# Optimization experiments

Measured on AMD Instinct MI355X. Metric: run time of the kernel, lower is better.

## Reference

```python
import jax, jax.numpy as jnp
import numpy as np

B, C, H, W = 4, 256, 200, 200
N_ROIS = 2048
CROP = 7
NUM_CLASSES = 2
HID = 1024
FAN_IN = C * CROP * CROP


def _linear_params(key, fan_in, fan_out):
    s = 1.0 / np.sqrt(fan_in)
    kw, kb = jax.random.split(key)
    w = jax.random.uniform(kw, (fan_out, fan_in), jnp.float32, -s, s)
    b = jax.random.uniform(kb, (fan_out,), jnp.float32, -s, s)
    return w, b


def setup_inputs() -> dict:
    key = jax.random.key(0)
    ks = jax.random.split(key, 10)
    x = jax.random.normal(ks[0], (B, C, H, W), jnp.float32)
    # rois: (batch_idx, x1, y1, x2, y2) in feature-map coords, sizes ~4-22px
    bi = jax.random.randint(ks[1], (N_ROIS,), 0, B).astype(jnp.float32)
    x1 = jax.random.uniform(ks[2], (N_ROIS,)) * (W - 24)
    y1 = jax.random.uniform(ks[3], (N_ROIS,)) * (H - 24)
    x2 = x1 + 4.0 + jax.random.uniform(ks[4], (N_ROIS,)) * 18.0
    y2 = y1 + 4.0 + jax.random.uniform(ks[5], (N_ROIS,)) * 18.0
    rpn_rois = jnp.stack([bi, x1, y1, x2, y2], axis=1)
    w1, b1 = _linear_params(ks[6], FAN_IN, HID)
    w2, b2 = _linear_params(ks[7], HID, HID)
    wc, bc = _linear_params(ks[8], HID, NUM_CLASSES)
    wb, bb = _linear_params(ks[9], HID, NUM_CLASSES * 4)
    return {"x": x, "rpn_rois": rpn_rois, "w1": w1, "b1": b1,
            "w2": w2, "b2": b2, "wc": wc, "bc": bc, "wb": wb, "bb": bb}


def roi_align(x, rois):
    """Per-ROI bilinear crop (RoIAlign, 1 sample/bin). x:[B,C,H,W], rois:[N,5] -> [N, C*CROP*CROP]."""
    n = rois.shape[0]
    b = rois[:, 0].astype(jnp.int32)
    rx1, ry1, rx2, ry2 = rois[:, 1], rois[:, 2], rois[:, 3], rois[:, 4]
    bw = (rx2 - rx1) / CROP
    bh = (ry2 - ry1) / CROP
    c = jnp.arange(CROP, dtype=jnp.float32) + 0.5  # bin centers
    sx = rx1[:, None] + c[None, :] * bw[:, None]   # [N, CROP]
    sy = ry1[:, None] + c[None, :] * bh[:, None]   # [N, CROP]
    P = CROP * CROP
    px = jnp.broadcast_to(sx[:, None, :], (n, CROP, CROP)).reshape(n, P)
    py = jnp.broadcast_to(sy[:, :, None], (n, CROP, CROP)).reshape(n, P)
    px = jnp.clip(px, 0.0, W - 1)
    py = jnp.clip(py, 0.0, H - 1)
    x0 = jnp.floor(px).astype(jnp.int32)
    y0 = jnp.floor(py).astype(jnp.int32)
    x1i = jnp.minimum(x0 + 1, W - 1)
    y1i = jnp.minimum(y0 + 1, H - 1)
    wx = (px - x0.astype(px.dtype))[..., None]  # [N,P,1]
    wy = (py - y0.astype(py.dtype))[..., None]
    be = jnp.broadcast_to(b[:, None], (n, P))
    v00 = x[be, :, y0, x0]   # [N,P,C] irregular gathers
    v01 = x[be, :, y0, x1i]
    v10 = x[be, :, y1i, x0]
    v11 = x[be, :, y1i, x1i]
    val = (v00 * (1 - wy) * (1 - wx) + v01 * (1 - wy) * wx
           + v10 * wy * (1 - wx) + v11 * wy * wx)        # [N,P,C]
    return val.transpose(0, 2, 1).reshape(n, C * P)       # channel-major flatten, matches torch


def reference(x, rpn_rois, w1, b1, w2, b2, wc, bc, wb, bb):
    crops = roi_align(x, rpn_rois)                 # [N, C*cs*cs]
    h = jax.nn.relu(crops @ w1.T + b1)             # fc1
    h = jax.nn.relu(h @ w2.T + b2)                 # fc2
    rcnn_class_logits = h @ wc.T + bc              # [N, num_classes]
    rcnn_bbox = h @ wb.T + bb                      # [N, num_classes*4]
    return (rcnn_class_logits, rcnn_bbox)
```

## Files before the change

### kernel.cpp

```cpp
#include <hip/hip_runtime.h>

#define NROI  2048
#define CCH   256
#define IMH   200
#define IMW   200
#define CROP  7
#define PP    49
#define FANIN 12544
#define HID   1024

typedef _Float16 f16x8 __attribute__((ext_vector_type(8)));
typedef _Float16 f16x4 __attribute__((ext_vector_type(4)));
typedef __attribute__((ext_vector_type(4))) float f32x4;

__device__ __forceinline__ void gload16(const void* g, void* l) {
    __builtin_amdgcn_global_load_lds(
        (const __attribute__((address_space(1))) void*)g,
        (__attribute__((address_space(3))) void*)l, 16, 0, 0);
}

__global__ __launch_bounds__(256) void transpose_f16(
    const float* __restrict__ x, _Float16* __restrict__ xT)
{
    __shared__ _Float16 t[100][258];

    const int half = blockIdx.x;
    const int h    = blockIdx.y;
    const int b    = blockIdx.z;
    const int c    = threadIdx.x;

    const float* src = x + ((size_t)(b * CCH + c) * IMH + h) * IMW + half * 100;
#pragma unroll
    for (int i = 0; i < 25; ++i) {
        const float4 v = *(const float4*)(src + i * 4);
        t[i * 4 + 0][c] = (_Float16)v.x;
        t[i * 4 + 1][c] = (_Float16)v.y;
        t[i * 4 + 2][c] = (_Float16)v.z;
        t[i * 4 + 3][c] = (_Float16)v.w;
    }
    __syncthreads();

    _Float16* dst = xT + ((size_t)(b * IMH + h) * IMW + half * 100) * CCH;
    const int wq = threadIdx.x >> 5;
    const int l32 = threadIdx.x & 31;
#pragma unroll
    for (int r = 0; r < 13; ++r) {
        const int w = r * 8 + wq;
        if (w < 100)
            *(f16x8*)(dst + (size_t)w * CCH + l32 * 8) =
                *(const f16x8*)&t[w][l32 * 8];
    }
}

__global__ __launch_bounds__(256) void roi_gather_kernel(
    const _Float16* __restrict__ xT, const float* __restrict__ rois,
    _Float16* __restrict__ crops)
{
    const int n    = blockIdx.x;
    const int wave = threadIdx.x >> 6;
    const int lane = threadIdx.x & 63;

    const int   b   = (int)rois[(size_t)n * 5 + 0];
    const float rx1 = rois[(size_t)n * 5 + 1];
    const float ry1 = rois[(size_t)n * 5 + 2];
    const float rx2 = rois[(size_t)n * 5 + 3];
    const float ry2 = rois[(size_t)n * 5 + 4];
    const float bw = (rx2 - rx1) / 7.0f;
    const float bh = (ry2 - ry1) / 7.0f;

    const _Float16* xb = xT + (size_t)b * (IMH * IMW * CCH);
    _Float16* crow = crops + (size_t)n * FANIN;

    for (int p = wave; p < PP; p += 4) {
        const int i = p / 7;
        const int j = p - i * 7;
        float px = __fadd_rn(rx1, __fmul_rn((float)j + 0.5f, bw));
        float py = __fadd_rn(ry1, __fmul_rn((float)i + 0.5f, bh));
        px = fminf(fmaxf(px, 0.0f), (float)(IMW - 1));
        py = fminf(fmaxf(py, 0.0f), (float)(IMH - 1));
        const float fx = floorf(px), fy = floorf(py);
        const int x0 = (int)fx, y0 = (int)fy;
        const int dxo = (min(x0 + 1, IMW - 1) - x0) * CCH;
        const int dyo = (min(y0 + 1, IMH - 1) - y0) * (IMW * CCH);
        const float wx = px - fx, wy = py - fy;

        const _Float16* cb = xb + (size_t)(y0 * IMW + x0) * CCH + lane * 4;
        const f16x4 A = *(const f16x4*)(cb);
        const f16x4 B = *(const f16x4*)(cb + dxo);
        const f16x4 C = *(const f16x4*)(cb + dyo);
        const f16x4 D = *(const f16x4*)(cb + dyo + dxo);

        f16x4 o;
#pragma unroll
        for (int e = 0; e < 4; ++e) {
            const float v00 = (float)A[e], v01 = (float)B[e];
            const float v10 = (float)C[e], v11 = (float)D[e];
            const float top = v00 + wx * (v01 - v00);
            const float bot = v10 + wx * (v11 - v10);
            o[e] = (_Float16)(top + wy * (bot - top));
        }
        *(f16x4*)(crow + p * CCH + lane * 4) = o;
    }
}

__global__ __launch_bounds__(256) void permute_w1_kernel(
    const float* __restrict__ w1, _Float16* __restrict__ w1P)
{
    __shared__ _Float16 row[FANIN];

    const int o   = blockIdx.x;
    const int tid = threadIdx.x;
    const float* src = w1 + (size_t)o * FANIN;

    for (int g = tid; g < FANIN / 4; g += 256) {
        const float4 v = *(const float4*)(src + g * 4);
        f16x4 f = {(_Float16)v.x, (_Float16)v.y, (_Float16)v.z, (_Float16)v.w};
        *(f16x4*)&row[g * 4] = f;
    }
    __syncthreads();

    _Float16* dst = w1P + (size_t)o * FANIN;
    for (int g = tid; g < FANIN; g += 256) {
        const int p = g >> 8;
        const int c = g & 255;
        dst[g] = row[c * PP + p];
    }
}

__global__ __launch_bounds__(256) void convert_f16(
    const float* __restrict__ w, _Float16* __restrict__ wF, int n4)
{
    for (int g = blockIdx.x * 256 + threadIdx.x; g < n4; g += gridDim.x * 256) {
        const float4 v = ((const float4*)w)[g];
        f16x4 o = {(_Float16)v.x, (_Float16)v.y, (_Float16)v.z, (_Float16)v.w};
        ((f16x4*)wF)[g] = o;
    }
}

__global__ __launch_bounds__(512, 1) void gemm_f16_256(
    const _Float16* __restrict__ A, const _Float16* __restrict__ B,
    float* __restrict__ P, int M, int N, int K, int kLen)
{
    __shared__ _Float16 lds[2][2][256][64];

    const int flat = blockIdx.x;
    const int xcd  = flat & 7;
    const int idx  = flat >> 3;
    const int bn4  = xcd & 3;
    const int half = xcd >> 2;
    const int bm8  = half * 4 + (idx & 3);
    const int z    = idx >> 2;

    const int tid  = threadIdx.x;
    const int wave = tid >> 6;
    const int lane = tid & 63;
    const int bm = bm8 * 256;
    const int bn = bn4 * 256;
    const int kBase = z * kLen;
    const int wr = wave >> 1;
    const int wc = wave & 1;

    f32x4 acc[4][8];
#pragma unroll
    for (int i = 0; i < 4; ++i)
#pragma unroll
        for (int j = 0; j < 8; ++j) acc[i][j] = (f32x4){0.f, 0.f, 0.f, 0.f};

    const int r_st = wave * 32 + (lane >> 3);
    const int s_st = ((lane & 7) ^ ((lane >> 4) & 3)) * 8;
    const _Float16* gA = A + (size_t)(bm + r_st) * K + kBase + s_st;
    const _Float16* gB = B + (size_t)(bn + r_st) * K + kBase + s_st;
    const size_t rstep8 = (size_t)8 * K;

    const int li = lane & 15;
    const int hi = lane >> 4;
    const int swb = (li >> 1) & 3;

    {
        _Float16* dA = &lds[0][0][wave * 32][0];
        _Float16* dB = &lds[0][1][wave * 32][0];
#pragma unroll
        for (int ck = 0; ck < 4; ++ck) {
            gload16(gA + ck * rstep8, dA + ck * 512);
            gload16(gB + ck * rstep8, dB + ck * 512);
        }
    }
    __syncthreads();

    int cur = 0;
    for (int kt = 0; kt < kLen; kt += 64) {
        if (kt + 64 < kLen) {
            _Float16* dA = &lds[cur ^ 1][0][wave * 32][0];
            _Float16* dB = &lds[cur ^ 1][1][wave * 32][0];
#pragma unroll
            for (int ck = 0; ck < 4; ++ck) {
                gload16(gA + kt + 64 + ck * rstep8, dA + ck * 512);
                gload16(gB + kt + 64 + ck * rstep8, dB + ck * 512);
            }
        }

#pragma unroll
        for (int kk = 0; kk < 2; ++kk) {
            const int sw = (((kk << 2) | hi) ^ swb) * 8;
            f16x8 a[4], b[8];
#pragma unroll
            for (int m = 0; m < 4; ++m)
                a[m] = *(const f16x8*)&lds[cur][0][wr * 64 + m * 16 + li][sw];
#pragma unroll
            for (int n = 0; n < 8; ++n)
                b[n] = *(const f16x8*)&lds[cur][1][wc * 128 + n * 16 + li][sw];
#pragma unroll
            for (int m = 0; m < 4; ++m)
#pragma unroll
                for (int n = 0; n < 8; ++n)
                    acc[m][n] = __builtin_amdgcn_mfma_f32_16x16x32_f16(a[m], b[n], acc[m][n], 0, 0, 0);
        }
        __syncthreads();
        cur ^= 1;
    }

    float* Pz = P + (size_t)z * M * N;
#pragma unroll
    for (int m = 0; m < 4; ++m)
#pragma unroll
        for (int n = 0; n < 8; ++n) {
            const int col = bn + wc * 128 + n * 16 + li;
#pragma unroll
            for (int e = 0; e < 4; ++e) {
                const int row = bm + wr * 64 + m * 16 + hi * 4 + e;
                Pz[(size_t)row * N + col] = acc[m][n][e];
            }
        }
}

__global__ __launch_bounds__(256, 2) void gemm_f16(
    const _Float16* __restrict__ A, const _Float16* __restrict__ B,
    float* __restrict__ P, int M, int N, int K, int kLen)
{
    __shared__ _Float16 lds[2][2][128][64];

    const int tid  = threadIdx.x;
    const int wave = tid >> 6;
    const int lane = tid & 63;
    const int bm = blockIdx.y * 128;
    const int bn = blockIdx.x * 128;
    const int kBase = blockIdx.z * kLen;
    const int wr = wave >> 1, wc = wave & 1;

    f32x4 acc[4][4];
#pragma unroll
    for (int i = 0; i < 4; ++i)
#pragma unroll
        for (int j = 0; j < 4; ++j) acc[i][j] = (f32x4){0.f, 0.f, 0.f, 0.f};

    const int r_st = wave * 32 + (lane >> 3);
    const int s_st = ((lane & 7) ^ ((lane >> 4) & 3)) * 8;
    const _Float16* gA = A + (size_t)(bm + r_st) * K + kBase + s_st;
    const _Float16* gB = B + (size_t)(bn + r_st) * K + kBase + s_st;
    const size_t rstep8 = (size_t)8 * K;

    const int li = lane & 15;
    const int hi = lane >> 4;
    const int swb = (li >> 1) & 3;

    {
        _Float16* dA = &lds[0][0][wave * 32][0];
        _Float16* dB = &lds[0][1][wave * 32][0];
#pragma unroll
        for (int ck = 0; ck < 4; ++ck) {
            gload16(gA + ck * rstep8, dA + ck * 512);
            gload16(gB + ck * rstep8, dB + ck * 512);
        }
    }
    __syncthreads();

    int cur = 0;
    for (int kt = 0; kt < kLen; kt += 64) {
        if (kt + 64 < kLen) {
            _Float16* dA = &lds[cur ^ 1][0][wave * 32][0];
            _Float16* dB = &lds[cur ^ 1][1][wave * 32][0];
#pragma unroll
            for (int ck = 0; ck < 4; ++ck) {
                gload16(gA + kt + 64 + ck * rstep8, dA + ck * 512);
                gload16(gB + kt + 64 + ck * rstep8, dB + ck * 512);
            }
        }

#pragma unroll
        for (int kk = 0; kk < 2; ++kk) {
            const int sw = (((kk << 2) | hi) ^ swb) * 8;
            f16x8 a[4], b[4];
#pragma unroll
            for (int m = 0; m < 4; ++m)
                a[m] = *(const f16x8*)&lds[cur][0][wr * 64 + m * 16 + li][sw];
#pragma unroll
            for (int n = 0; n < 4; ++n)
                b[n] = *(const f16x8*)&lds[cur][1][wc * 64 + n * 16 + li][sw];
#pragma unroll
            for (int m = 0; m < 4; ++m)
#pragma unroll
                for (int n = 0; n < 4; ++n)
                    acc[m][n] = __builtin_amdgcn_mfma_f32_16x16x32_f16(a[m], b[n], acc[m][n], 0, 0, 0);
        }
        __syncthreads();
        cur ^= 1;
    }

    float* Pz = P + (size_t)blockIdx.z * M * N;
#pragma unroll
    for (int m = 0; m < 4; ++m)
#pragma unroll
        for (int n = 0; n < 4; ++n) {
            const int col = bn + wc * 64 + n * 16 + li;
#pragma unroll
            for (int e = 0; e < 4; ++e) {
                const int row = bm + wr * 64 + m * 16 + hi * 4 + e;
                Pz[(size_t)row * N + col] = acc[m][n][e];
            }
        }
}

__global__ __launch_bounds__(256) void combine_relu_f16(
    const float* __restrict__ P, int Z, const float* __restrict__ bias,
    _Float16* __restrict__ H)
{
    const int g = blockIdx.x * 256 + threadIdx.x;
    const size_t MN4 = (size_t)NROI * HID / 4;
    float4 s = ((const float4*)P)[g];
    for (int z = 1; z < Z; ++z) {
        const float4 p = ((const float4*)P)[z * MN4 + g];
        s.x += p.x; s.y += p.y; s.z += p.z; s.w += p.w;
    }
    const float4 bv = *(const float4*)(bias + (g & 255) * 4);
    f16x4 o = {(_Float16)fmaxf(s.x + bv.x, 0.0f),
               (_Float16)fmaxf(s.y + bv.y, 0.0f),
               (_Float16)fmaxf(s.z + bv.z, 0.0f),
               (_Float16)fmaxf(s.w + bv.w, 0.0f)};
    ((f16x4*)H)[g] = o;
}

__global__ __launch_bounds__(256) void combine_relu_f32(
    const float* __restrict__ P, int Z, const float* __restrict__ bias,
    float* __restrict__ H)
{
    const int g = blockIdx.x * 256 + threadIdx.x;
    const size_t MN4 = (size_t)NROI * HID / 4;
    float4 s = ((const float4*)P)[g];
    for (int z = 1; z < Z; ++z) {
        const float4 p = ((const float4*)P)[z * MN4 + g];
        s.x += p.x; s.y += p.y; s.z += p.z; s.w += p.w;
    }
    const float4 bv = *(const float4*)(bias + (g & 255) * 4);
    float4 r;
    r.x = fmaxf(s.x + bv.x, 0.0f);
    r.y = fmaxf(s.y + bv.y, 0.0f);
    r.z = fmaxf(s.z + bv.z, 0.0f);
    r.w = fmaxf(s.w + bv.w, 0.0f);
    ((float4*)H)[g] = r;
}

__global__ __launch_bounds__(256) void heads_kernel(
    const float* __restrict__ h2,
    const float* __restrict__ wc, const float* __restrict__ bc,
    const float* __restrict__ wb, const float* __restrict__ bb,
    float* __restrict__ out)
{
    const int gw   = (blockIdx.x * 256 + threadIdx.x) >> 6;
    const int lane = threadIdx.x & 63;
    const float* hrow = h2 + (size_t)gw * HID;

    float4 h[4];
#pragma unroll
    for (int j = 0; j < 4; ++j)
        h[j] = *(const float4*)(hrow + lane * 16 + j * 4);

    float keep = 0.0f;
#pragma unroll
    for (int o = 0; o < 10; ++o) {
        const float* wrow = (o < 2) ? (wc + (size_t)o * HID)
                                    : (wb + (size_t)(o - 2) * HID);
        float acc = 0.0f;
#pragma unroll
        for (int j = 0; j < 4; ++j) {
            const float4 w4 = *(const float4*)(wrow + lane * 16 + j * 4);
            acc += h[j].x * w4.x + h[j].y * w4.y + h[j].z * w4.z + h[j].w * w4.w;
        }
#pragma unroll
        for (int s = 32; s; s >>= 1) acc += __shfl_xor(acc, s, 64);
        if (lane == o) keep = acc;
    }
    if (lane < 2)        out[gw * 2 + lane] = keep + bc[lane];
    else if (lane < 10)  out[NROI * 2 + gw * 8 + (lane - 2)] = keep + bb[lane - 2];
}

extern "C" void kernel_launch(void* const* d_in, const int* in_sizes, int n_in,
                              void* d_out, int out_size, void* d_ws, size_t ws_size,
                              hipStream_t stream)
{
    const float* x    = (const float*)d_in[0];
    const float* rois = (const float*)d_in[1];
    const float* w1   = (const float*)d_in[2];
    const float* b1   = (const float*)d_in[3];
    const float* w2   = (const float*)d_in[4];
    const float* b2   = (const float*)d_in[5];
    const float* wc   = (const float*)d_in[6];
    const float* bc   = (const float*)d_in[7];
    const float* wb   = (const float*)d_in[8];
    const float* bb   = (const float*)d_in[9];
    float* out = (float*)d_out;

    char* ws = (char*)d_ws;
    const size_t CRB = (size_t)NROI * FANIN * 2;
    const size_t W1B = (size_t)HID * FANIN * 2;
    const size_t W2B = (size_t)HID * HID * 2;
    const size_t PB  = (size_t)NROI * HID * 4;
    const size_t HB  = (size_t)NROI * HID * 2;
    const size_t XTB = (size_t)4 * IMH * IMW * CCH * 2;

    const int Z1 = 7;
    const int Z2 = 4;

    size_t off = 0;
    _Float16* cropsP = (_Float16*)(ws + off); off += CRB;
    _Float16* w1P    = (_Float16*)(ws + off); off += W1B;
    _Float16* w2F    = (_Float16*)(ws + off); off += W2B;
    float*    P      = (float*)(ws + off);    off += (size_t)Z1 * PB;
    _Float16* h1F    = (_Float16*)(ws + off); off += HB;
    _Float16* xT     = (_Float16*)(ws + off); off += XTB;
    float*    h2     = P;

    permute_w1_kernel<<<HID, 256, 0, stream>>>(w1, w1P);
    convert_f16<<<1024, 256, 0, stream>>>(w2, w2F, HID * HID / 4);

    transpose_f16<<<dim3(2, IMH, 4), 256, 0, stream>>>(x, xT);

    roi_gather_kernel<<<NROI, 256, 0, stream>>>(xT, rois, cropsP);

    gemm_f16_256<<<224, 512, 0, stream>>>(
        cropsP, w1P, P, NROI, HID, FANIN, FANIN / Z1);
    combine_relu_f16<<<(NROI * HID / 4) / 256, 256, 0, stream>>>(P, Z1, b1, h1F);

    gemm_f16<<<dim3(HID / 128, NROI / 128, Z2), 256, 0, stream>>>(
        h1F, w2F, P, NROI, HID, HID, HID / Z2);
    combine_relu_f32<<<(NROI * HID / 4) / 256, 256, 0, stream>>>(P, Z2, b2, h2);

    heads_kernel<<<NROI / 4, 256, 0, stream>>>(h2, wc, bc, wb, bb, out);
}
```

Measured before the change: 216.7 us.

## Merge prep kernels and store split-K partials in fp16 to cut traffic

Folds the x transpose, the w1 permute and the w2 conversion into one launch that dispatches on block index, replacing three launches. Split-K partial sums are now written by both GEMMs and read by the combine kernels as fp16 instead of fp32, halving partial-buffer traffic, and the combine kernels now handle 8 elements per thread. Split-K for fc2 drops from 4 to 2, and h2 reuses the xT buffer. Rounding partials to fp16 adds precision loss and some risk of overflow. The merged prep kernel reserves about 51.6 KB of shared memory for every block, which may reduce occupancy for the transpose and conversion blocks.

```diff
diff --git a/kernel.cpp b/kernel.cpp
--- a/kernel.cpp
+++ b/kernel.cpp
@@ -19,36 +19,70 @@
         (__attribute__((address_space(3))) void*)l, 16, 0, 0);
 }
 
-__global__ __launch_bounds__(256) void transpose_f16(
-    const float* __restrict__ x, _Float16* __restrict__ xT)
-{
-    __shared__ _Float16 t[100][258];
-
-    const int half = blockIdx.x;
-    const int h    = blockIdx.y;
-    const int b    = blockIdx.z;
-    const int c    = threadIdx.x;
-
-    const float* src = x + ((size_t)(b * CCH + c) * IMH + h) * IMW + half * 100;
-#pragma unroll
-    for (int i = 0; i < 25; ++i) {
-        const float4 v = *(const float4*)(src + i * 4);
-        t[i * 4 + 0][c] = (_Float16)v.x;
-        t[i * 4 + 1][c] = (_Float16)v.y;
-        t[i * 4 + 2][c] = (_Float16)v.z;
-        t[i * 4 + 3][c] = (_Float16)v.w;
-    }
-    __syncthreads();
-
-    _Float16* dst = xT + ((size_t)(b * IMH + h) * IMW + half * 100) * CCH;
-    const int wq = threadIdx.x >> 5;
-    const int l32 = threadIdx.x & 31;
-#pragma unroll
-    for (int r = 0; r < 13; ++r) {
-        const int w = r * 8 + wq;
-        if (w < 100)
-            *(f16x8*)(dst + (size_t)w * CCH + l32 * 8) =
-                *(const f16x8*)&t[w][l32 * 8];
+__global__ __launch_bounds__(256) void prep_all(
+    const float* __restrict__ x, _Float16* __restrict__ xT,
+    const float* __restrict__ w1, _Float16* __restrict__ w1P,
+    const float* __restrict__ w2, _Float16* __restrict__ w2F)
+{
+    __shared__ char smem[51600];
+    const int bid = blockIdx.x;
+    const int tid = threadIdx.x;
+
+    if (bid < 1600) {
+        typedef _Float16 Row258[258];
+        Row258* t = (Row258*)smem;
+        const int b    = bid / 400;
+        const int rem  = bid - b * 400;
+        const int h    = rem >> 1;
+        const int half = rem & 1;
+        const int c    = tid;
+
+        const float* src = x + ((size_t)(b * CCH + c) * IMH + h) * IMW + half * 100;
+#pragma unroll
+        for (int i = 0; i < 25; ++i) {
+            const float4 v = *(const float4*)(src + i * 4);
+            t[i * 4 + 0][c] = (_Float16)v.x;
+            t[i * 4 + 1][c] = (_Float16)v.y;
+            t[i * 4 + 2][c] = (_Float16)v.z;
+            t[i * 4 + 3][c] = (_Float16)v.w;
+        }
+        __syncthreads();
+
+        _Float16* dst = xT + ((size_t)(b * IMH + h) * IMW + half * 100) * CCH;
+        const int wq = tid >> 5;
+        const int l32 = tid & 31;
+#pragma unroll
+        for (int r = 0; r < 13; ++r) {
+            const int w = r * 8 + wq;
+            if (w < 100)
+                *(f16x8*)(dst + (size_t)w * CCH + l32 * 8) =
+                    *(const f16x8*)&t[w][l32 * 8];
+        }
+    } else if (bid < 2624) {
+        _Float16* row = (_Float16*)smem;
+        const int o = bid - 1600;
+        const float* src = w1 + (size_t)o * FANIN;
+
+        for (int g = tid; g < FANIN / 4; g += 256) {
+            const float4 v = *(const float4*)(src + g * 4);
+            f16x4 f = {(_Float16)v.x, (_Float16)v.y, (_Float16)v.z, (_Float16)v.w};
+            *(f16x4*)&row[g * 4] = f;
+        }
+        __syncthreads();
+
+        _Float16* dst = w1P + (size_t)o * FANIN;
+        for (int g = tid; g < FANIN; g += 256) {
+            const int p = g >> 8;
+            const int c = g & 255;
+            dst[g] = row[c * PP + p];
+        }
+    } else {
+        const int cb = bid - 2624;
+        for (int g = cb * 256 + tid; g < HID * HID / 4; g += 64 * 256) {
+            const float4 v = ((const float4*)w2)[g];
+            f16x4 o = {(_Float16)v.x, (_Float16)v.y, (_Float16)v.z, (_Float16)v.w};
+            ((f16x4*)w2F)[g] = o;
+        }
     }
 }
 
@@ -103,43 +137,9 @@
     }
 }
 
-__global__ __launch_bounds__(256) void permute_w1_kernel(
-    const float* __restrict__ w1, _Float16* __restrict__ w1P)
-{
-    __shared__ _Float16 row[FANIN];
-
-    const int o   = blockIdx.x;
-    const int tid = threadIdx.x;
-    const float* src = w1 + (size_t)o * FANIN;
-
-    for (int g = tid; g < FANIN / 4; g += 256) {
-        const float4 v = *(const float4*)(src + g * 4);
-        f16x4 f = {(_Float16)v.x, (_Float16)v.y, (_Float16)v.z, (_Float16)v.w};
-        *(f16x4*)&row[g * 4] = f;
-    }
-    __syncthreads();
-
-    _Float16* dst = w1P + (size_t)o * FANIN;
-    for (int g = tid; g < FANIN; g += 256) {
-        const int p = g >> 8;
-        const int c = g & 255;
-        dst[g] = row[c * PP + p];
-    }
-}
-
-__global__ __launch_bounds__(256) void convert_f16(
-    const float* __restrict__ w, _Float16* __restrict__ wF, int n4)
-{
-    for (int g = blockIdx.x * 256 + threadIdx.x; g < n4; g += gridDim.x * 256) {
-        const float4 v = ((const float4*)w)[g];
-        f16x4 o = {(_Float16)v.x, (_Float16)v.y, (_Float16)v.z, (_Float16)v.w};
-        ((f16x4*)wF)[g] = o;
-    }
-}
-
 __global__ __launch_bounds__(512, 1) void gemm_f16_256(
     const _Float16* __restrict__ A, const _Float16* __restrict__ B,
-    float* __restrict__ P, int M, int N, int K, int kLen)
+    _Float16* __restrict__ P, int M, int N, int K, int kLen)
 {
     __shared__ _Float16 lds[2][2][256][64];
 
@@ -219,7 +219,7 @@
         cur ^= 1;
     }
 
-    float* Pz = P + (size_t)z * M * N;
+    _Float16* Pz = P + (size_t)z * M * N;
 #pragma unroll
     for (int m = 0; m < 4; ++m)
 #pragma unroll
@@ -228,14 +228,14 @@
 #pragma unroll
             for (int e = 0; e < 4; ++e) {
                 const int row = bm + wr * 64 + m * 16 + hi * 4 + e;
-                Pz[(size_t)row * N + col] = acc[m][n][e];
+                Pz[(size_t)row * N + col] = (_Float16)acc[m][n][e];
             }
         }
 }
 
 __global__ __launch_bounds__(256, 2) void gemm_f16(
     const _Float16* __restrict__ A, const _Float16* __restrict__ B,
-    float* __restrict__ P, int M, int N, int K, int kLen)
+    _Float16* __restrict__ P, int M, int N, int K, int kLen)
 {
     __shared__ _Float16 lds[2][2][128][64];
 
@@ -306,7 +306,7 @@
         cur ^= 1;
     }
 
-    float* Pz = P + (size_t)blockIdx.z * M * N;
+    _Float16* Pz = P + (size_t)blockIdx.z * M * N;
 #pragma unroll
     for (int m = 0; m < 4; ++m)
 #pragma unroll
@@ -315,48 +315,64 @@
 #pragma unroll
             for (int e = 0; e < 4; ++e) {
                 const int row = bm + wr * 64 + m * 16 + hi * 4 + e;
-                Pz[(size_t)row * N + col] = acc[m][n][e];
+                Pz[(size_t)row * N + col] = (_Float16)acc[m][n][e];
             }
         }
 }
 
 __global__ __launch_bounds__(256) void combine_relu_f16(
-    const float* __restrict__ P, int Z, const float* __restrict__ bias,
+    const _Float16* __restrict__ P, int Z, const float* __restrict__ bias,
     _Float16* __restrict__ H)
 {
     const int g = blockIdx.x * 256 + threadIdx.x;
-    const size_t MN4 = (size_t)NROI * HID / 4;
-    float4 s = ((const float4*)P)[g];
-    for (int z = 1; z < Z; ++z) {
-        const float4 p = ((const float4*)P)[z * MN4 + g];
-        s.x += p.x; s.y += p.y; s.z += p.z; s.w += p.w;
-    }
-    const float4 bv = *(const float4*)(bias + (g & 255) * 4);
-    f16x4 o = {(_Float16)fmaxf(s.x + bv.x, 0.0f),
-               (_Float16)fmaxf(s.y + bv.y, 0.0f),
-               (_Float16)fmaxf(s.z + bv.z, 0.0f),
-               (_Float16)fmaxf(s.w + bv.w, 0.0f)};
-    ((f16x4*)H)[g] = o;
+    const size_t MN8 = (size_t)NROI * HID / 8;
+    float s[8] = {0, 0, 0, 0, 0, 0, 0, 0};
+    for (int z = 0; z < Z; ++z) {
+        const f16x8 p = ((const f16x8*)P)[z * MN8 + g];
+#pragma unroll
+        for (int e = 0; e < 8; ++e) s[e] += (float)p[e];
+    }
+    const int col = (g * 8) & (HID - 1);
+    const float4 b0 = *(const float4*)(bias + col);
+    const float4 b1 = *(const float4*)(bias + col + 4);
+    f16x8 o;
+    o[0] = (_Float16)fmaxf(s[0] + b0.x, 0.0f);
+    o[1] = (_Float16)fmaxf(s[1] + b0.y, 0.0f);
+    o[2] = (_Float16)fmaxf(s[2] + b0.z, 0.0f);
+    o[3] = (_Float16)fmaxf(s[3] + b0.w, 0.0f);
+    o[4] = (_Float16)fmaxf(s[4] + b1.x, 0.0f);
+    o[5] = (_Float16)fmaxf(s[5] + b1.y, 0.0f);
+    o[6] = (_Float16)fmaxf(s[6] + b1.z, 0.0f);
+    o[7] = (_Float16)fmaxf(s[7] + b1.w, 0.0f);
+    ((f16x8*)H)[g] = o;
 }
 
 __global__ __launch_bounds__(256) void combine_relu_f32(
-    const float* __restrict__ P, int Z, const float* __restrict__ bias,
+    const _Float16* __restrict__ P, int Z, const float* __restrict__ bias,
     float* __restrict__ H)
 {
     const int g = blockIdx.x * 256 + threadIdx.x;
-    const size_t MN4 = (size_t)NROI * HID / 4;
-    float4 s = ((const float4*)P)[g];
-    for (int z = 1; z < Z; ++z) {
-        const float4 p = ((const float4*)P)[z * MN4 + g];
-        s.x += p.x; s.y += p.y; s.z += p.z; s.w += p.w;
-    }
-    const float4 bv = *(const float4*)(bias + (g & 255) * 4);
-    float4 r;
-    r.x = fmaxf(s.x + bv.x, 0.0f);
-    r.y = fmaxf(s.y + bv.y, 0.0f);
-    r.z = fmaxf(s.z + bv.z, 0.0f);
-    r.w = fmaxf(s.w + bv.w, 0.0f);
-    ((float4*)H)[g] = r;
+    const size_t MN8 = (size_t)NROI * HID / 8;
+    float s[8] = {0, 0, 0, 0, 0, 0, 0, 0};
+    for (int z = 0; z < Z; ++z) {
+        const f16x8 p = ((const f16x8*)P)[z * MN8 + g];
+#pragma unroll
+        for (int e = 0; e < 8; ++e) s[e] += (float)p[e];
+    }
+    const int col = (g * 8) & (HID - 1);
+    const float4 b0 = *(const float4*)(bias + col);
+    const float4 b1 = *(const float4*)(bias + col + 4);
+    float4 r0, r1;
+    r0.x = fmaxf(s[0] + b0.x, 0.0f);
+    r0.y = fmaxf(s[1] + b0.y, 0.0f);
+    r0.z = fmaxf(s[2] + b0.z, 0.0f);
+    r0.w = fmaxf(s[3] + b0.w, 0.0f);
+    r1.x = fmaxf(s[4] + b1.x, 0.0f);
+    r1.y = fmaxf(s[5] + b1.y, 0.0f);
+    r1.z = fmaxf(s[6] + b1.z, 0.0f);
+    r1.w = fmaxf(s[7] + b1.w, 0.0f);
+    ((float4*)H)[g * 2]     = r0;
+    ((float4*)H)[g * 2 + 1] = r1;
 }
 
 __global__ __launch_bounds__(256) void heads_kernel(
@@ -413,36 +429,33 @@
     const size_t CRB = (size_t)NROI * FANIN * 2;
     const size_t W1B = (size_t)HID * FANIN * 2;
     const size_t W2B = (size_t)HID * HID * 2;
-    const size_t PB  = (size_t)NROI * HID * 4;
+    const size_t PB  = (size_t)NROI * HID * 2;
     const size_t HB  = (size_t)NROI * HID * 2;
     const size_t XTB = (size_t)4 * IMH * IMW * CCH * 2;
 
     const int Z1 = 7;
-    const int Z2 = 4;
+    const int Z2 = 2;
 
     size_t off = 0;
     _Float16* cropsP = (_Float16*)(ws + off); off += CRB;
     _Float16* w1P    = (_Float16*)(ws + off); off += W1B;
     _Float16* w2F    = (_Float16*)(ws + off); off += W2B;
-    float*    P      = (float*)(ws + off);    off += (size_t)Z1 * PB;
+    _Float16* P      = (_Float16*)(ws + off); off += (size_t)Z1 * PB;
     _Float16* h1F    = (_Float16*)(ws + off); off += HB;
     _Float16* xT     = (_Float16*)(ws + off); off += XTB;
-    float*    h2     = P;
-
-    permute_w1_kernel<<<HID, 256, 0, stream>>>(w1, w1P);
-    convert_f16<<<1024, 256, 0, stream>>>(w2, w2F, HID * HID / 4);
-
-    transpose_f16<<<dim3(2, IMH, 4), 256, 0, stream>>>(x, xT);
+    float*    h2     = (float*)xT;
+
+    prep_all<<<2688, 256, 0, stream>>>(x, xT, w1, w1P, w2, w2F);
 
     roi_gather_kernel<<<NROI, 256, 0, stream>>>(xT, rois, cropsP);
 
     gemm_f16_256<<<224, 512, 0, stream>>>(
         cropsP, w1P, P, NROI, HID, FANIN, FANIN / Z1);
-    combine_relu_f16<<<(NROI * HID / 4) / 256, 256, 0, stream>>>(P, Z1, b1, h1F);
+    combine_relu_f16<<<(NROI * HID / 8) / 256, 256, 0, stream>>>(P, Z1, b1, h1F);
 
     gemm_f16<<<dim3(HID / 128, NROI / 128, Z2), 256, 0, stream>>>(
         h1F, w2F, P, NROI, HID, HID, HID / Z2);
-    combine_relu_f32<<<(NROI * HID / 4) / 256, 256, 0, stream>>>(P, Z2, b2, h2);
+    combine_relu_f32<<<(NROI * HID / 8) / 256, 256, 0, stream>>>(P, Z2, b2, h2);
 
     heads_kernel<<<NROI / 4, 256, 0, stream>>>(h2, wc, bc, wb, bb, out);
 }
```

New measurement: 196.9 us. 1.1x faster.
